# Optimization experiments

Measured on AMD Instinct MI355X. Metric: run time of the kernel, lower is better.

The kernel has to match this reference:

```python
import jax, jax.numpy as jnp
import numpy as np

HID, H, QR, KVR, DN, DR, DV = 2048, 20, 768, 512, 192, 64, 256
HEAD_DIM = DN + DR  # 256
EPS = 1e-5
THETA = 1000000.0
SCALE = 1.0 / np.sqrt(HEAD_DIM)


def rmsnorm(x, w):
    rms = jnp.sqrt(jnp.mean(x * x, axis=-1, keepdims=True) + EPS)
    return x / rms * w


def rope_apply(x, positions):
    # x: [B,S,H,DR], positions: [B,S] int
    inv_freq = 1.0 / (THETA ** (jnp.arange(0, DR, 2, dtype=jnp.float32) / DR))  # [DR/2]
    freqs = positions.astype(jnp.float32)[..., None] * inv_freq  # [B,S,DR/2]
    cos = jnp.cos(freqs)[:, :, None, :]  # [B,S,1,DR/2]
    sin = jnp.sin(freqs)[:, :, None, :]
    x1, x2 = x[..., ::2], x[..., 1::2]
    return jnp.concatenate([x1 * cos - x2 * sin, x1 * sin + x2 * cos], axis=-1)


def setup_inputs() -> dict:
    key = jax.random.key(0)
    ks = jax.random.split(key, 7)
    B, S = 1, 2048
    return {
        "x": jax.random.normal(ks[0], (B, S, HID), dtype=jnp.float32),
        "positions": jnp.tile(jnp.arange(S, dtype=jnp.int32)[None, :], (B, 1)),
        "q_a_w": jax.random.normal(ks[1], (QR, HID), dtype=jnp.float32) * 0.02,
        "q_b_w": jax.random.normal(ks[2], (H * HEAD_DIM, QR), dtype=jnp.float32) * 0.02,
        "kv_a_w": jax.random.normal(ks[3], (KVR + DR, HID), dtype=jnp.float32) * 0.02,
        "kv_b_w": jax.random.normal(ks[4], (H * (DN + DV), KVR), dtype=jnp.float32) * 0.02,
        "o_w": jax.random.normal(ks[5], (HID, H * DV), dtype=jnp.float32) * 0.02,
        "q_a_ln_w": jnp.ones((QR,), dtype=jnp.float32),
        "kv_a_ln_w": jnp.ones((KVR,), dtype=jnp.float32),
    }


def reference(x, positions, q_a_w, q_b_w, kv_a_w, kv_b_w, o_w, q_a_ln_w, kv_a_ln_w):
    B, S, _ = x.shape
    # Q: LoRA down -> RMSNorm -> up
    q = rmsnorm(x @ q_a_w.T, q_a_ln_w) @ q_b_w.T  # [B,S,H*HEAD_DIM]
    q = q.reshape(B, S, H, HEAD_DIM)
    # KV: compressed projection, split lora / rope-pe parts
    kv_c = x @ kv_a_w.T  # [B,S,KVR+DR]
    kv_lora, k_rope_pe = kv_c[..., :KVR], kv_c[..., KVR:]
    kv_exp = rmsnorm(kv_lora, kv_a_ln_w) @ kv_b_w.T  # [B,S,H*(DN+DV)]
    kv_exp = kv_exp.reshape(B, S, H, DN + DV)
    k_nope, v = kv_exp[..., :DN], kv_exp[..., DN:]
    k_rope = jnp.broadcast_to(k_rope_pe[:, :, None, :], (B, S, H, DR))
    q_nope, q_rope = q[..., :DN], q[..., DN:]
    q_rope = rope_apply(q_rope, positions)
    k_rope = rope_apply(k_rope, positions)
    qf = jnp.concatenate([q_nope, q_rope], axis=-1)  # [B,S,H,HEAD_DIM]
    kf = jnp.concatenate([k_nope, k_rope], axis=-1)
    # attention: manual matmul-softmax-matmul
    attn = jnp.einsum("bqhd,bkhd->bhqk", qf, kf) * SCALE
    attn = jax.nn.softmax(attn, axis=-1)
    out = jnp.einsum("bhqk,bkhd->bqhd", attn, v).reshape(B, S, H * DV)
    return out @ o_w.T
```

## Files before the change

### kernel.cpp

```cpp
#include <hip/hip_runtime.h>
#include <hip/hip_bf16.h>

#define HID 2048
#define NH 20
#define QR 768
#define KVR 512
#define DN 192
#define DR 64
#define DV 256
#define HD 256
#define S_LEN 2048
#define HKV 448
#define KV_N (NH * HKV)
#define Q_N (NH * HD)
#define O_N (NH * DV)
#define KVA_N (KVR + DR)
#define KVAP 640
#define QKVA (QR + KVAP)

typedef short bf16x8 __attribute__((ext_vector_type(8)));
typedef short bf16x4 __attribute__((ext_vector_type(4)));
typedef float f32x4 __attribute__((ext_vector_type(4)));

__device__ inline short f2bs(float f) {
  __hip_bfloat16 h = __float2bfloat16(f);
  return *reinterpret_cast<short*>(&h);
}
__device__ inline float bs2f(short s) {
  __hip_bfloat16 h = *reinterpret_cast<__hip_bfloat16*>(&s);
  return __bfloat162float(h);
}

__device__ inline void gload16(const void* g, void* l) {
  __builtin_amdgcn_global_load_lds((const __attribute__((address_space(1))) void*)g,
                                   (__attribute__((address_space(3))) void*)l, 16, 0, 0);
}

#define WAIT_VM0() asm volatile("s_waitcnt vmcnt(0)" ::: "memory")

__global__ void f2b_kernel(const float* __restrict__ in, short* __restrict__ out, size_t n8) {
  size_t i = (size_t)blockIdx.x * blockDim.x + threadIdx.x;
  size_t stride = (size_t)gridDim.x * blockDim.x;
  for (; i < n8; i += stride) {
    f32x4 a = *(const f32x4*)(in + i * 8);
    f32x4 b = *(const f32x4*)(in + i * 8 + 4);
    bf16x8 r;
    r[0] = f2bs(a[0]); r[1] = f2bs(a[1]); r[2] = f2bs(a[2]); r[3] = f2bs(a[3]);
    r[4] = f2bs(b[0]); r[5] = f2bs(b[1]); r[6] = f2bs(b[2]); r[7] = f2bs(b[3]);
    *(bf16x8*)(out + i * 8) = r;
  }
}

template <int OUT_BF16>
__global__ __launch_bounds__(256) void gemm128(const short* __restrict__ A,
                                               const short* __restrict__ B,
                                               void* __restrict__ Cp,
                                               int M, int N, int K) {
  __shared__ alignas(16) short As[128 * 64];
  __shared__ alignas(16) short Bs[128 * 64];
  int tid = threadIdx.x;
  int w = tid >> 6, l = tid & 63;
  int lr = l & 15, lg = l >> 4;
  int wr = w >> 1, wc = w & 1;
  int row0 = blockIdx.y * 128, col0 = blockIdx.x * 128;
  f32x4 acc[4][4] = {};
  for (int k0 = 0; k0 < K; k0 += 64) {
    if (k0) __syncthreads();
#pragma unroll
    for (int p = 0; p < 4; ++p) {
      int c = p * 256 + tid;
      int row = c >> 3;
      int sb = ((c & 7) * 16) ^ ((row & 7) << 4);
      gload16((const char*)A + ((size_t)(row0 + row) * K + k0) * 2 + sb, (char*)As + c * 16);
      gload16((const char*)B + ((size_t)(col0 + row) * K + k0) * 2 + sb, (char*)Bs + c * 16);
    }
    __syncthreads();
    bf16x8 af[4][2], bf[4][2];
#pragma unroll
    for (int m = 0; m < 4; ++m)
#pragma unroll
      for (int kk = 0; kk < 2; ++kk) {
        int ra = wr * 64 + m * 16 + lr;
        int rb = wc * 64 + m * 16 + lr;
        int cb = kk * 64 + lg * 16;
        af[m][kk] = *(const bf16x8*)((const char*)As + ra * 128 + (cb ^ ((ra & 7) << 4)));
        bf[m][kk] = *(const bf16x8*)((const char*)Bs + rb * 128 + (cb ^ ((rb & 7) << 4)));
      }
#pragma unroll
    for (int m = 0; m < 4; ++m)
#pragma unroll
      for (int n = 0; n < 4; ++n) {
        acc[m][n] = __builtin_amdgcn_mfma_f32_16x16x32_bf16(af[m][0], bf[n][0], acc[m][n], 0, 0, 0);
        acc[m][n] = __builtin_amdgcn_mfma_f32_16x16x32_bf16(af[m][1], bf[n][1], acc[m][n], 0, 0, 0);
      }
  }
#pragma unroll
  for (int m = 0; m < 4; ++m)
#pragma unroll
    for (int n = 0; n < 4; ++n)
#pragma unroll
      for (int r = 0; r < 4; ++r) {
        int row = row0 + wr * 64 + m * 16 + lg * 4 + r;
        int col = col0 + wc * 64 + n * 16 + lr;
        if (OUT_BF16)
          ((short*)Cp)[(size_t)row * N + col] = f2bs(acc[m][n][r]);
        else
          ((float*)Cp)[(size_t)row * N + col] = acc[m][n][r];
      }
}

__global__ __launch_bounds__(256) void gemm64(const short* __restrict__ A,
                                              const short* __restrict__ B,
                                              float* __restrict__ C,
                                              int M, int N, int K) {
  __shared__ alignas(16) short As[64 * 64];
  __shared__ alignas(16) short Bs[128 * 64];
  int tid = threadIdx.x;
  int w = tid >> 6, l = tid & 63;
  int lr = l & 15, lg = l >> 4;
  int wr = w >> 1, wc = w & 1;
  int row0 = blockIdx.y * 64, col0 = blockIdx.x * 128;
  f32x4 acc[2][4] = {};
  for (int k0 = 0; k0 < K; k0 += 64) {
    if (k0) __syncthreads();
#pragma unroll
    for (int p = 0; p < 2; ++p) {
      int c = p * 256 + tid;
      int row = c >> 3;
      int sb = ((c & 7) * 16) ^ ((row & 7) << 4);
      gload16((const char*)A + ((size_t)(row0 + row) * K + k0) * 2 + sb, (char*)As + c * 16);
    }
#pragma unroll
    for (int p = 0; p < 4; ++p) {
      int c = p * 256 + tid;
      int row = c >> 3;
      int sb = ((c & 7) * 16) ^ ((row & 7) << 4);
      gload16((const char*)B + ((size_t)(col0 + row) * K + k0) * 2 + sb, (char*)Bs + c * 16);
    }
    __syncthreads();
    bf16x8 af[2][2], bf[4][2];
#pragma unroll
    for (int m = 0; m < 2; ++m)
#pragma unroll
      for (int kk = 0; kk < 2; ++kk) {
        int ra = wr * 32 + m * 16 + lr;
        int cb = kk * 64 + lg * 16;
        af[m][kk] = *(const bf16x8*)((const char*)As + ra * 128 + (cb ^ ((ra & 7) << 4)));
      }
#pragma unroll
    for (int n = 0; n < 4; ++n)
#pragma unroll
      for (int kk = 0; kk < 2; ++kk) {
        int rb = wc * 64 + n * 16 + lr;
        int cb = kk * 64 + lg * 16;
        bf[n][kk] = *(const bf16x8*)((const char*)Bs + rb * 128 + (cb ^ ((rb & 7) << 4)));
      }
#pragma unroll
    for (int m = 0; m < 2; ++m)
#pragma unroll
      for (int n = 0; n < 4; ++n) {
        acc[m][n] = __builtin_amdgcn_mfma_f32_16x16x32_bf16(af[m][0], bf[n][0], acc[m][n], 0, 0, 0);
        acc[m][n] = __builtin_amdgcn_mfma_f32_16x16x32_bf16(af[m][1], bf[n][1], acc[m][n], 0, 0, 0);
      }
  }
#pragma unroll
  for (int m = 0; m < 2; ++m)
#pragma unroll
    for (int n = 0; n < 4; ++n)
#pragma unroll
      for (int r = 0; r < 4; ++r) {
        int row = row0 + wr * 32 + m * 16 + lg * 4 + r;
        int col = col0 + wc * 64 + n * 16 + lr;
        C[(size_t)row * N + col] = acc[m][n][r];
      }
}

__global__ __launch_bounds__(256) void rmsnorm_kernel(const float* __restrict__ in,
                                                      const float* __restrict__ w,
                                                      short* __restrict__ out,
                                                      int N, int in_stride, int out_stride) {
  int row = blockIdx.x;
  const float* x = in + (size_t)row * in_stride;
  float ss = 0.f;
  for (int i = threadIdx.x * 4; i < N; i += 1024) {
    f32x4 v = *(const f32x4*)(x + i);
    ss += v[0] * v[0] + v[1] * v[1] + v[2] * v[2] + v[3] * v[3];
  }
#pragma unroll
  for (int off = 32; off >= 1; off >>= 1) ss += __shfl_down(ss, off);
  __shared__ float red[4];
  if ((threadIdx.x & 63) == 0) red[threadIdx.x >> 6] = ss;
  __syncthreads();
  float tot = red[0] + red[1] + red[2] + red[3];
  float sc = rsqrtf(tot / (float)N + 1e-5f);
  short* o = out + (size_t)row * out_stride;
  for (int i = threadIdx.x * 4; i < N; i += 1024) {
    f32x4 v = *(const f32x4*)(x + i);
    f32x4 g = *(const f32x4*)(w + i);
    bf16x4 r;
    r[0] = f2bs(v[0] * sc * g[0]); r[1] = f2bs(v[1] * sc * g[1]);
    r[2] = f2bs(v[2] * sc * g[2]); r[3] = f2bs(v[3] * sc * g[3]);
    *(bf16x4*)(o + i) = r;
  }
}

__global__ void rope_table_kernel(const int* __restrict__ pos, float* __restrict__ ct,
                                  float* __restrict__ st) {
  int s = blockIdx.x * blockDim.x + threadIdx.x;
  if (s >= S_LEN) return;
  double p = (double)pos[s];
  for (int d = 0; d < 32; ++d) {
    double invf = exp(-((double)(2 * d) / 64.0) * log(1.0e6));
    double a = p * invf;
    ct[s * 32 + d] = (float)cos(a);
    st[s * 32 + d] = (float)sin(a);
  }
}

__global__ void rope_q_kernel(short* __restrict__ q, const float* __restrict__ ct,
                              const float* __restrict__ st) {
  int idx = blockIdx.x * blockDim.x + threadIdx.x;
  if (idx >= S_LEN * NH) return;
  int s = idx / NH, h = idx % NH;
  short* p = q + (size_t)s * Q_N + h * HD + DN;
  bf16x8 v[8];
#pragma unroll
  for (int j = 0; j < 8; ++j) v[j] = *(const bf16x8*)(p + j * 8);
  float x[64];
#pragma unroll
  for (int j = 0; j < 8; ++j)
#pragma unroll
    for (int k = 0; k < 8; ++k) x[j * 8 + k] = bs2f(v[j][k]);
  const float* c = ct + s * 32;
  const float* sn = st + s * 32;
  bf16x8 o[8];
#pragma unroll
  for (int d = 0; d < 32; ++d) {
    float cd = c[d], sd = sn[d];
    float x1 = x[2 * d], x2 = x[2 * d + 1];
    o[d >> 3][d & 7] = f2bs(x1 * cd - x2 * sd);
    o[4 + (d >> 3)][d & 7] = f2bs(x1 * sd + x2 * cd);
  }
#pragma unroll
  for (int j = 0; j < 8; ++j) *(bf16x8*)(p + j * 8) = o[j];
}

__global__ void rope_k_kernel(const float* __restrict__ base, const float* __restrict__ ct,
                              const float* __restrict__ st, short* __restrict__ kr) {
  int s = blockIdx.x * blockDim.x + threadIdx.x;
  if (s >= S_LEN) return;
  const float* xp = base + (size_t)s * QKVA;
  float x[64];
#pragma unroll
  for (int j = 0; j < 16; ++j) {
    f32x4 v = *(const f32x4*)(xp + j * 4);
    x[j * 4] = v[0]; x[j * 4 + 1] = v[1]; x[j * 4 + 2] = v[2]; x[j * 4 + 3] = v[3];
  }
  const float* c = ct + s * 32;
  const float* sn = st + s * 32;
  bf16x8 o[8];
#pragma unroll
  for (int d = 0; d < 32; ++d) {
    float cd = c[d], sd = sn[d];
    float x1 = x[2 * d], x2 = x[2 * d + 1];
    o[d >> 3][d & 7] = f2bs(x1 * cd - x2 * sd);
    o[4 + (d >> 3)][d & 7] = f2bs(x1 * sd + x2 * cd);
  }
  short* kp = kr + s * 64;
#pragma unroll
  for (int j = 0; j < 8; ++j) *(bf16x8*)(kp + j * 8) = o[j];
}

__global__ void kc_build(const short* __restrict__ kvx, const short* __restrict__ kr,
                         short* __restrict__ kc) {
  int idx = blockIdx.x * 256 + threadIdx.x;
  int h = idx >> 16;
  int r = idx & 65535;
  int s = r >> 5, c = r & 31;
  const short* src = (c < 24) ? kvx + (size_t)s * KV_N + h * HKV + c * 8
                              : kr + (size_t)s * 64 + (c - 24) * 8;
  *(bf16x8*)(kc + ((size_t)h * S_LEN + s) * HD + c * 8) = *(const bf16x8*)src;
}

__global__ __launch_bounds__(256) void vtrans(const short* __restrict__ kvx,
                                              short* __restrict__ vtg) {
  __shared__ short tile[64][65];
  int s0 = blockIdx.x * 64, d0 = blockIdx.y * 64, h = blockIdx.z;
  int tid = threadIdx.x;
#pragma unroll
  for (int p = 0; p < 2; ++p) {
    int s = p * 32 + (tid >> 3), dc = (tid & 7) * 8;
    bf16x8 v = *(const bf16x8*)(kvx + (size_t)(s0 + s) * KV_N + h * HKV + DN + d0 + dc);
#pragma unroll
    for (int j = 0; j < 8; ++j) tile[s][dc + j] = v[j];
  }
  __syncthreads();
#pragma unroll
  for (int p = 0; p < 2; ++p) {
    int d = p * 32 + (tid >> 3), sc = (tid & 7) * 8;
    bf16x4 a, b;
#pragma unroll
    for (int j = 0; j < 4; ++j) a[j] = tile[sc + j][d];
#pragma unroll
    for (int j = 0; j < 4; ++j) b[j] = tile[sc + 4 + j][d];
    int q1 = sc & 31, q2 = q1 + 4;
    int p1 = (q1 < 16) ? (q1 >> 2) * 8 : ((q1 - 16) >> 2) * 8 + 4;
    int p2 = (q2 < 16) ? (q2 >> 2) * 8 : ((q2 - 16) >> 2) * 8 + 4;
    int s = ((d & 15) >> 1) & 3;
    p1 = ((((p1 >> 3) ^ s)) << 3) | (p1 & 7);
    p2 = ((((p2 >> 3) ^ s)) << 3) | (p2 & 7);
    size_t rowbase = ((size_t)h * DV + d0 + d) * S_LEN + s0 + (sc & ~31);
    *(bf16x4*)(vtg + rowbase + p1) = a;
    *(bf16x4*)(vtg + rowbase + p2) = b;
  }
}

__global__ __launch_bounds__(256, 4) void attn8(const short* __restrict__ q,
                                                const short* __restrict__ kc,
                                                const short* __restrict__ vtg,
                                                short* __restrict__ out) {
  __shared__ alignas(16) short ks[2][32 * 256];
  __shared__ alignas(16) short vt[2][256 * 32];
  int bid = blockIdx.x;
  int swz = (bid & 7) * 80 + (bid >> 3);
  int h = swz >> 5, qblk = swz & 31;
  int tid = threadIdx.x;
  int w = tid >> 6, l = tid & 63;
  int lr = l & 15, lg = l >> 4;

  const char* kch = (const char*)(kc + (size_t)h * S_LEN * HD);
  const short* vth = vtg + (size_t)h * DV * S_LEN;

  int qrow = qblk * 64 + w * 16 + lr;
  const short* qbase = q + (size_t)qrow * Q_N + h * HD;
  bf16x8 qf[8];
#pragma unroll
  for (int kk = 0; kk < 8; ++kk) {
    bf16x8 v = *(const bf16x8*)(qbase + kk * 32 + lg * 8);
#pragma unroll
    for (int j = 0; j < 8; ++j) v[j] = f2bs(bs2f(v[j]) * 0.0625f);
    qf[kk] = v;
  }

  f32x4 acc[16] = {};
  float m = -3e38f;
  float lsum = 0.f;

  auto stage_k = [&](int buf, int key0) {
#pragma unroll
    for (int p = 0; p < 4; ++p) {
      int c = p * 256 + tid;
      int row = c >> 5;
      int sb = ((c & 31) * 16) ^ ((row & 7) << 4);
      gload16(kch + (size_t)(key0 + row) * 512 + sb, (char*)ks[buf] + c * 16);
    }
  };
  auto stage_v = [&](int buf, int key0) {
#pragma unroll
    for (int p = 0; p < 4; ++p) {
      int c = p * 256 + tid;
      int d = c >> 2, slot = c & 3;
      gload16(vth + (size_t)d * S_LEN + key0 + slot * 8, (char*)vt[buf] + c * 16);
    }
  };

  stage_k(0, 0);
  stage_v(0, 0);
  WAIT_VM0();
  __builtin_amdgcn_s_barrier();

  int sxor = (lr >> 1) & 3;

  for (int kb = 0; kb < S_LEN / 32; ++kb) {
    int cur = kb & 1;
    int key0 = kb * 32;
    if (kb + 1 < S_LEN / 32) {
      stage_k(cur ^ 1, key0 + 32);
      stage_v(cur ^ 1, key0 + 32);
    }

    f32x4 s0 = {}, s1 = {};
    __builtin_amdgcn_s_setprio(1);
#pragma unroll
    for (int kk = 0; kk < 8; ++kk) {
      int cb = kk * 64 + lg * 16;
      int sw = (lr & 7) << 4;
      bf16x8 k0 = *(const bf16x8*)((const char*)ks[cur] + lr * 512 + (cb ^ sw));
      bf16x8 k1 = *(const bf16x8*)((const char*)ks[cur] + (16 + lr) * 512 + (cb ^ sw));
      s0 = __builtin_amdgcn_mfma_f32_16x16x32_bf16(k0, qf[kk], s0, 0, 0, 0);
      s1 = __builtin_amdgcn_mfma_f32_16x16x32_bf16(k1, qf[kk], s1, 0, 0, 0);
    }
    __builtin_amdgcn_s_setprio(0);

    float mx = fmaxf(fmaxf(fmaxf(s0[0], s0[1]), fmaxf(s0[2], s0[3])),
                     fmaxf(fmaxf(s1[0], s1[1]), fmaxf(s1[2], s1[3])));
    mx = fmaxf(mx, __shfl_xor(mx, 16));
    mx = fmaxf(mx, __shfl_xor(mx, 32));
    bool grow = mx > m + 8.f;
    if (__any((int)grow)) {
      float mn = fmaxf(m, mx);
      float co = __expf(m - mn);
      m = mn;
      lsum *= co;
      float c0 = __shfl(co, (l & 48) | (lg * 4 + 0));
      float c1 = __shfl(co, (l & 48) | (lg * 4 + 1));
      float c2 = __shfl(co, (l & 48) | (lg * 4 + 2));
      float c3 = __shfl(co, (l & 48) | (lg * 4 + 3));
#pragma unroll
      for (int t = 0; t < 16; ++t) {
        acc[t][0] *= c0; acc[t][1] *= c1; acc[t][2] *= c2; acc[t][3] *= c3;
      }
    }
    float e0 = __expf(s0[0] - m), e1 = __expf(s0[1] - m);
    float e2 = __expf(s0[2] - m), e3 = __expf(s0[3] - m);
    float e4 = __expf(s1[0] - m), e5 = __expf(s1[1] - m);
    float e6 = __expf(s1[2] - m), e7 = __expf(s1[3] - m);
    float ts = ((e0 + e1) + (e2 + e3)) + ((e4 + e5) + (e6 + e7));
    ts += __shfl_xor(ts, 16);
    ts += __shfl_xor(ts, 32);
    lsum += ts;
    bf16x8 pa;
    pa[0] = f2bs(e0); pa[1] = f2bs(e1); pa[2] = f2bs(e2); pa[3] = f2bs(e3);
    pa[4] = f2bs(e4); pa[5] = f2bs(e5); pa[6] = f2bs(e6); pa[7] = f2bs(e7);

    __builtin_amdgcn_s_setprio(1);
#pragma unroll
    for (int t = 0; t < 16; ++t) {
      int d = t * 16 + lr;
      bf16x8 vf = *(const bf16x8*)((const char*)vt[cur] + d * 64 + ((lg ^ sxor) << 4));
      acc[t] = __builtin_amdgcn_mfma_f32_16x16x32_bf16(pa, vf, acc[t], 0, 0, 0);
    }
    __builtin_amdgcn_s_setprio(0);

    WAIT_VM0();
    __builtin_amdgcn_s_barrier();
  }

  float inv = 1.f / lsum;
  float i0 = __shfl(inv, (l & 48) | (lg * 4 + 0));
  float i1 = __shfl(inv, (l & 48) | (lg * 4 + 1));
  float i2 = __shfl(inv, (l & 48) | (lg * 4 + 2));
  float i3 = __shfl(inv, (l & 48) | (lg * 4 + 3));
#pragma unroll
  for (int t = 0; t < 16; ++t) {
    int row = qblk * 64 + w * 16 + lg * 4;
    int col = h * DV + t * 16 + lr;
    out[(size_t)(row + 0) * O_N + col] = f2bs(acc[t][0] * i0);
    out[(size_t)(row + 1) * O_N + col] = f2bs(acc[t][1] * i1);
    out[(size_t)(row + 2) * O_N + col] = f2bs(acc[t][2] * i2);
    out[(size_t)(row + 3) * O_N + col] = f2bs(acc[t][3] * i3);
  }
}

extern "C" void kernel_launch(void* const* d_in, const int* in_sizes, int n_in,
                              void* d_out, int out_size, void* d_ws, size_t ws_size,
                              hipStream_t stream) {
  const float* x       = (const float*)d_in[0];
  const int*   pos     = (const int*)d_in[1];
  const float* q_a_w   = (const float*)d_in[2];
  const float* q_b_w   = (const float*)d_in[3];
  const float* kv_a_w  = (const float*)d_in[4];
  const float* kv_b_w  = (const float*)d_in[5];
  const float* o_w     = (const float*)d_in[6];
  const float* q_a_ln  = (const float*)d_in[7];
  const float* kv_a_ln = (const float*)d_in[8];
  float* out = (float*)d_out;

  char* p = (char*)d_ws;
  auto alloc = [&](size_t bytes) {
    char* r = p;
    p += (bytes + 255) & ~(size_t)255;
    return r;
  };
  short* xb    = (short*)alloc((size_t)S_LEN * HID * 2);
  short* wcat  = (short*)alloc((size_t)QKVA * HID * 2);
  short* qbw   = (short*)alloc((size_t)Q_N * QR * 2);
  short* kvbw  = (short*)alloc((size_t)KV_N * KVR * 2);
  short* ow    = (short*)alloc((size_t)HID * O_N * 2);
  float* qkv   = (float*)alloc((size_t)S_LEN * QKVA * 4);
  short* q_ln  = (short*)alloc((size_t)S_LEN * QR * 2);
  short* qbuf  = (short*)alloc((size_t)S_LEN * Q_N * 2);
  short* kv_ln = (short*)alloc((size_t)S_LEN * KVR * 2);
  short* kvx   = (short*)alloc((size_t)S_LEN * KV_N * 2);
  short* kr    = (short*)alloc((size_t)S_LEN * 64 * 2);
  float* ct    = (float*)alloc((size_t)S_LEN * 32 * 4);
  float* st    = (float*)alloc((size_t)S_LEN * 32 * 4);
  short* ao    = (short*)alloc((size_t)S_LEN * O_N * 2);
  short* kcb   = (short*)alloc((size_t)NH * S_LEN * HD * 2);
  short* vtg   = (short*)alloc((size_t)NH * DV * S_LEN * 2);
  (void)ws_size; (void)n_in; (void)in_sizes; (void)out_size;

  auto cvt = [&](const float* in, short* o, size_t n) {
    size_t n8 = n / 8;
    size_t blocks = (n8 + 255) / 256;
    if (blocks > 2048) blocks = 2048;
    f2b_kernel<<<dim3((unsigned)blocks), dim3(256), 0, stream>>>(in, o, n8);
  };
  cvt(x, xb, (size_t)S_LEN * HID);
  cvt(q_a_w, wcat, (size_t)QR * HID);
  cvt(kv_a_w, wcat + (size_t)QR * HID, (size_t)KVA_N * HID);
  hipMemsetAsync(wcat + (size_t)(QR + KVA_N) * HID, 0, (size_t)(KVAP - KVA_N) * HID * 2, stream);
  cvt(q_b_w, qbw, (size_t)Q_N * QR);
  cvt(kv_b_w, kvbw, (size_t)KV_N * KVR);
  cvt(o_w, ow, (size_t)HID * O_N);

  dim3 blk(256);
  gemm64<<<dim3(QKVA / 128, S_LEN / 64), blk, 0, stream>>>(xb, wcat, qkv, S_LEN, QKVA, HID);
  rmsnorm_kernel<<<dim3(S_LEN), blk, 0, stream>>>(qkv, q_a_ln, q_ln, QR, QKVA, QR);
  rmsnorm_kernel<<<dim3(S_LEN), blk, 0, stream>>>(qkv + QR, kv_a_ln, kv_ln, KVR, QKVA, KVR);
  gemm128<1><<<dim3(Q_N / 128, S_LEN / 128), blk, 0, stream>>>(q_ln, qbw, qbuf, S_LEN, Q_N, QR);
  gemm128<1><<<dim3(KV_N / 128, S_LEN / 128), blk, 0, stream>>>(kv_ln, kvbw, kvx, S_LEN, KV_N, KVR);
  rope_table_kernel<<<dim3(S_LEN / 256), blk, 0, stream>>>(pos, ct, st);
  rope_q_kernel<<<dim3((S_LEN * NH + 255) / 256), blk, 0, stream>>>(qbuf, ct, st);
  rope_k_kernel<<<dim3(S_LEN / 256), blk, 0, stream>>>(qkv + QR + KVR, ct, st, kr);
  kc_build<<<dim3(NH * S_LEN * 32 / 256), blk, 0, stream>>>(kvx, kr, kcb);
  vtrans<<<dim3(S_LEN / 64, DV / 64, NH), blk, 0, stream>>>(kvx, vtg);
  attn8<<<dim3(NH * S_LEN / 64), blk, 0, stream>>>(qbuf, kcb, vtg, ao);
  gemm64<<<dim3(HID / 128, S_LEN / 64), blk, 0, stream>>>(ao, ow, out, S_LEN, HID, O_N);
}
```

Measured before the change: 441.3 us.

## Process two query tiles per wave in attention to reuse staged K/V

Each wave now handles 32 query rows as two independent 16-row tiles, sharing every K and V fragment read from LDS across both. This halves the block count and the K/V staging traffic per query, and doubles the MFMA work per LDS load. In exchange, register use roughly doubles (two accumulator sets and Q fragment sets), launch bounds drop to 2 blocks per CU, and fewer blocks may balance worse across CUs.

```diff
diff --git a/kernel.cpp b/kernel.cpp
--- a/kernel.cpp
+++ b/kernel.cpp
@@ -315,15 +315,15 @@
   }
 }
 
-__global__ __launch_bounds__(256, 4) void attn8(const short* __restrict__ q,
-                                                const short* __restrict__ kc,
-                                                const short* __restrict__ vtg,
-                                                short* __restrict__ out) {
+__global__ __launch_bounds__(256, 2) void attn10(const short* __restrict__ q,
+                                                 const short* __restrict__ kc,
+                                                 const short* __restrict__ vtg,
+                                                 short* __restrict__ out) {
   __shared__ alignas(16) short ks[2][32 * 256];
   __shared__ alignas(16) short vt[2][256 * 32];
   int bid = blockIdx.x;
-  int swz = (bid & 7) * 80 + (bid >> 3);
-  int h = swz >> 5, qblk = swz & 31;
+  int swz = (bid & 7) * 40 + (bid >> 3);
+  int h = swz >> 4, qblk = swz & 15;
   int tid = threadIdx.x;
   int w = tid >> 6, l = tid & 63;
   int lr = l & 15, lg = l >> 4;
@@ -331,20 +331,26 @@
   const char* kch = (const char*)(kc + (size_t)h * S_LEN * HD);
   const short* vth = vtg + (size_t)h * DV * S_LEN;
 
-  int qrow = qblk * 64 + w * 16 + lr;
-  const short* qbase = q + (size_t)qrow * Q_N + h * HD;
-  bf16x8 qf[8];
+  int qrowA = qblk * 128 + w * 32 + lr;
+  const short* qbA = q + (size_t)qrowA * Q_N + h * HD;
+  const short* qbB = qbA + (size_t)16 * Q_N;
+  bf16x8 qfA[8], qfB[8];
 #pragma unroll
   for (int kk = 0; kk < 8; ++kk) {
-    bf16x8 v = *(const bf16x8*)(qbase + kk * 32 + lg * 8);
-#pragma unroll
-    for (int j = 0; j < 8; ++j) v[j] = f2bs(bs2f(v[j]) * 0.0625f);
-    qf[kk] = v;
-  }
-
-  f32x4 acc[16] = {};
-  float m = -3e38f;
-  float lsum = 0.f;
+    bf16x8 va = *(const bf16x8*)(qbA + kk * 32 + lg * 8);
+    bf16x8 vb = *(const bf16x8*)(qbB + kk * 32 + lg * 8);
+#pragma unroll
+    for (int j = 0; j < 8; ++j) {
+      va[j] = f2bs(bs2f(va[j]) * 0.0625f);
+      vb[j] = f2bs(bs2f(vb[j]) * 0.0625f);
+    }
+    qfA[kk] = va;
+    qfB[kk] = vb;
+  }
+
+  f32x4 accA[16] = {}, accB[16] = {};
+  float mA = -3e38f, mB = -3e38f;
+  float lsA = 0.f, lsB = 0.f;
 
   auto stage_k = [&](int buf, int key0) {
 #pragma unroll
@@ -379,7 +385,7 @@
       stage_v(cur ^ 1, key0 + 32);
     }
 
-    f32x4 s0 = {}, s1 = {};
+    f32x4 s0A = {}, s1A = {}, s0B = {}, s1B = {};
     __builtin_amdgcn_s_setprio(1);
 #pragma unroll
     for (int kk = 0; kk < 8; ++kk) {
@@ -387,48 +393,84 @@
       int sw = (lr & 7) << 4;
       bf16x8 k0 = *(const bf16x8*)((const char*)ks[cur] + lr * 512 + (cb ^ sw));
       bf16x8 k1 = *(const bf16x8*)((const char*)ks[cur] + (16 + lr) * 512 + (cb ^ sw));
-      s0 = __builtin_amdgcn_mfma_f32_16x16x32_bf16(k0, qf[kk], s0, 0, 0, 0);
-      s1 = __builtin_amdgcn_mfma_f32_16x16x32_bf16(k1, qf[kk], s1, 0, 0, 0);
+      s0A = __builtin_amdgcn_mfma_f32_16x16x32_bf16(k0, qfA[kk], s0A, 0, 0, 0);
+      s1A = __builtin_amdgcn_mfma_f32_16x16x32_bf16(k1, qfA[kk], s1A, 0, 0, 0);
+      s0B = __builtin_amdgcn_mfma_f32_16x16x32_bf16(k0, qfB[kk], s0B, 0, 0, 0);
+      s1B = __builtin_amdgcn_mfma_f32_16x16x32_bf16(k1, qfB[kk], s1B, 0, 0, 0);
     }
     __builtin_amdgcn_s_setprio(0);
 
-    float mx = fmaxf(fmaxf(fmaxf(s0[0], s0[1]), fmaxf(s0[2], s0[3])),
-                     fmaxf(fmaxf(s1[0], s1[1]), fmaxf(s1[2], s1[3])));
-    mx = fmaxf(mx, __shfl_xor(mx, 16));
-    mx = fmaxf(mx, __shfl_xor(mx, 32));
-    bool grow = mx > m + 8.f;
-    if (__any((int)grow)) {
-      float mn = fmaxf(m, mx);
-      float co = __expf(m - mn);
-      m = mn;
-      lsum *= co;
-      float c0 = __shfl(co, (l & 48) | (lg * 4 + 0));
-      float c1 = __shfl(co, (l & 48) | (lg * 4 + 1));
-      float c2 = __shfl(co, (l & 48) | (lg * 4 + 2));
-      float c3 = __shfl(co, (l & 48) | (lg * 4 + 3));
-#pragma unroll
-      for (int t = 0; t < 16; ++t) {
-        acc[t][0] *= c0; acc[t][1] *= c1; acc[t][2] *= c2; acc[t][3] *= c3;
-      }
-    }
-    float e0 = __expf(s0[0] - m), e1 = __expf(s0[1] - m);
-    float e2 = __expf(s0[2] - m), e3 = __expf(s0[3] - m);
-    float e4 = __expf(s1[0] - m), e5 = __expf(s1[1] - m);
-    float e6 = __expf(s1[2] - m), e7 = __expf(s1[3] - m);
-    float ts = ((e0 + e1) + (e2 + e3)) + ((e4 + e5) + (e6 + e7));
-    ts += __shfl_xor(ts, 16);
-    ts += __shfl_xor(ts, 32);
-    lsum += ts;
-    bf16x8 pa;
-    pa[0] = f2bs(e0); pa[1] = f2bs(e1); pa[2] = f2bs(e2); pa[3] = f2bs(e3);
-    pa[4] = f2bs(e4); pa[5] = f2bs(e5); pa[6] = f2bs(e6); pa[7] = f2bs(e7);
+    bf16x8 paA, paB;
+    {
+      float mx = fmaxf(fmaxf(fmaxf(s0A[0], s0A[1]), fmaxf(s0A[2], s0A[3])),
+                       fmaxf(fmaxf(s1A[0], s1A[1]), fmaxf(s1A[2], s1A[3])));
+      mx = fmaxf(mx, __shfl_xor(mx, 16));
+      mx = fmaxf(mx, __shfl_xor(mx, 32));
+      bool grow = mx > mA + 8.f;
+      if (__any((int)grow)) {
+        float mn = fmaxf(mA, mx);
+        float co = __expf(mA - mn);
+        mA = mn;
+        lsA *= co;
+        float c0 = __shfl(co, (l & 48) | (lg * 4 + 0));
+        float c1 = __shfl(co, (l & 48) | (lg * 4 + 1));
+        float c2 = __shfl(co, (l & 48) | (lg * 4 + 2));
+        float c3 = __shfl(co, (l & 48) | (lg * 4 + 3));
+#pragma unroll
+        for (int t = 0; t < 16; ++t) {
+          accA[t][0] *= c0; accA[t][1] *= c1; accA[t][2] *= c2; accA[t][3] *= c3;
+        }
+      }
+      float e0 = __expf(s0A[0] - mA), e1 = __expf(s0A[1] - mA);
+      float e2 = __expf(s0A[2] - mA), e3 = __expf(s0A[3] - mA);
+      float e4 = __expf(s1A[0] - mA), e5 = __expf(s1A[1] - mA);
+      float e6 = __expf(s1A[2] - mA), e7 = __expf(s1A[3] - mA);
+      float ts = ((e0 + e1) + (e2 + e3)) + ((e4 + e5) + (e6 + e7));
+      ts += __shfl_xor(ts, 16);
+      ts += __shfl_xor(ts, 32);
+      lsA += ts;
+      paA[0] = f2bs(e0); paA[1] = f2bs(e1); paA[2] = f2bs(e2); paA[3] = f2bs(e3);
+      paA[4] = f2bs(e4); paA[5] = f2bs(e5); paA[6] = f2bs(e6); paA[7] = f2bs(e7);
+    }
+    {
+      float mx = fmaxf(fmaxf(fmaxf(s0B[0], s0B[1]), fmaxf(s0B[2], s0B[3])),
+                       fmaxf(fmaxf(s1B[0], s1B[1]), fmaxf(s1B[2], s1B[3])));
+      mx = fmaxf(mx, __shfl_xor(mx, 16));
+      mx = fmaxf(mx, __shfl_xor(mx, 32));
+      bool grow = mx > mB + 8.f;
+      if (__any((int)grow)) {
+        float mn = fmaxf(mB, mx);
+        float co = __expf(mB - mn);
+        mB = mn;
+        lsB *= co;
+        float c0 = __shfl(co, (l & 48) | (lg * 4 + 0));
+        float c1 = __shfl(co, (l & 48) | (lg * 4 + 1));
+        float c2 = __shfl(co, (l & 48) | (lg * 4 + 2));
+        float c3 = __shfl(co, (l & 48) | (lg * 4 + 3));
+#pragma unroll
+        for (int t = 0; t < 16; ++t) {
+          accB[t][0] *= c0; accB[t][1] *= c1; accB[t][2] *= c2; accB[t][3] *= c3;
+        }
+      }
+      float e0 = __expf(s0B[0] - mB), e1 = __expf(s0B[1] - mB);
+      float e2 = __expf(s0B[2] - mB), e3 = __expf(s0B[3] - mB);
+      float e4 = __expf(s1B[0] - mB), e5 = __expf(s1B[1] - mB);
+      float e6 = __expf(s1B[2] - mB), e7 = __expf(s1B[3] - mB);
+      float ts = ((e0 + e1) + (e2 + e3)) + ((e4 + e5) + (e6 + e7));
+      ts += __shfl_xor(ts, 16);
+      ts += __shfl_xor(ts, 32);
+      lsB += ts;
+      paB[0] = f2bs(e0); paB[1] = f2bs(e1); paB[2] = f2bs(e2); paB[3] = f2bs(e3);
+      paB[4] = f2bs(e4); paB[5] = f2bs(e5); paB[6] = f2bs(e6); paB[7] = f2bs(e7);
+    }
 
     __builtin_amdgcn_s_setprio(1);
 #pragma unroll
     for (int t = 0; t < 16; ++t) {
       int d = t * 16 + lr;
       bf16x8 vf = *(const bf16x8*)((const char*)vt[cur] + d * 64 + ((lg ^ sxor) << 4));
-      acc[t] = __builtin_amdgcn_mfma_f32_16x16x32_bf16(pa, vf, acc[t], 0, 0, 0);
+      accA[t] = __builtin_amdgcn_mfma_f32_16x16x32_bf16(paA, vf, accA[t], 0, 0, 0);
+      accB[t] = __builtin_amdgcn_mfma_f32_16x16x32_bf16(paB, vf, accB[t], 0, 0, 0);
     }
     __builtin_amdgcn_s_setprio(0);
 
@@ -436,19 +478,37 @@
     __builtin_amdgcn_s_barrier();
   }
 
-  float inv = 1.f / lsum;
-  float i0 = __shfl(inv, (l & 48) | (lg * 4 + 0));
-  float i1 = __shfl(inv, (l & 48) | (lg * 4 + 1));
-  float i2 = __shfl(inv, (l & 48) | (lg * 4 + 2));
-  float i3 = __shfl(inv, (l & 48) | (lg * 4 + 3));
-#pragma unroll
-  for (int t = 0; t < 16; ++t) {
-    int row = qblk * 64 + w * 16 + lg * 4;
-    int col = h * DV + t * 16 + lr;
-    out[(size_t)(row + 0) * O_N + col] = f2bs(acc[t][0] * i0);
-    out[(size_t)(row + 1) * O_N + col] = f2bs(acc[t][1] * i1);
-    out[(size_t)(row + 2) * O_N + col] = f2bs(acc[t][2] * i2);
-    out[(size_t)(row + 3) * O_N + col] = f2bs(acc[t][3] * i3);
+  {
+    float inv = 1.f / lsA;
+    float i0 = __shfl(inv, (l & 48) | (lg * 4 + 0));
+    float i1 = __shfl(inv, (l & 48) | (lg * 4 + 1));
+    float i2 = __shfl(inv, (l & 48) | (lg * 4 + 2));
+    float i3 = __shfl(inv, (l & 48) | (lg * 4 + 3));
+#pragma unroll
+    for (int t = 0; t < 16; ++t) {
+      int row = qblk * 128 + w * 32 + lg * 4;
+      int col = h * DV + t * 16 + lr;
+      out[(size_t)(row + 0) * O_N + col] = f2bs(accA[t][0] * i0);
+      out[(size_t)(row + 1) * O_N + col] = f2bs(accA[t][1] * i1);
+      out[(size_t)(row + 2) * O_N + col] = f2bs(accA[t][2] * i2);
+      out[(size_t)(row + 3) * O_N + col] = f2bs(accA[t][3] * i3);
+    }
+  }
+  {
+    float inv = 1.f / lsB;
+    float i0 = __shfl(inv, (l & 48) | (lg * 4 + 0));
+    float i1 = __shfl(inv, (l & 48) | (lg * 4 + 1));
+    float i2 = __shfl(inv, (l & 48) | (lg * 4 + 2));
+    float i3 = __shfl(inv, (l & 48) | (lg * 4 + 3));
+#pragma unroll
+    for (int t = 0; t < 16; ++t) {
+      int row = qblk * 128 + w * 32 + 16 + lg * 4;
+      int col = h * DV + t * 16 + lr;
+      out[(size_t)(row + 0) * O_N + col] = f2bs(accB[t][0] * i0);
+      out[(size_t)(row + 1) * O_N + col] = f2bs(accB[t][1] * i1);
+      out[(size_t)(row + 2) * O_N + col] = f2bs(accB[t][2] * i2);
+      out[(size_t)(row + 3) * O_N + col] = f2bs(accB[t][3] * i3);
+    }
   }
 }
 
@@ -515,6 +575,6 @@
   rope_k_kernel<<<dim3(S_LEN / 256), blk, 0, stream>>>(qkv + QR + KVR, ct, st, kr);
   kc_build<<<dim3(NH * S_LEN * 32 / 256), blk, 0, stream>>>(kvx, kr, kcb);
   vtrans<<<dim3(S_LEN / 64, DV / 64, NH), blk, 0, stream>>>(kvx, vtg);
-  attn8<<<dim3(NH * S_LEN / 64), blk, 0, stream>>>(qbuf, kcb, vtg, ao);
+  attn10<<<dim3(NH * S_LEN / 128), blk, 0, stream>>>(qbuf, kcb, vtg, ao);
   gemm64<<<dim3(HID / 128, S_LEN / 64), blk, 0, stream>>>(ao, ow, out, S_LEN, HID, O_N);
 }
```

Measured after the change: 386.7 us. -12.4%, faster.
